# Kernel optimization log

Measured on AMD Instinct MI355X. Metric: run time of the kernel, lower is better.

The kernel has to match this reference:

```python
import jax, jax.numpy as jnp
import numpy as np

N = 100_000          # nodes
E = 1_600_000        # directed edges (before self-loops)
IN_DIM, H1, H2, H3 = 128, 64, 64, 64
NEG_SLOPE = 0.2      # PyG GATConv default


def setup_inputs() -> dict:
    key = jax.random.key(0)
    ks = jax.random.split(key, 20)

    def glorot(k, shape):
        fan = shape[0] + shape[-1] if len(shape) > 1 else 1 + shape[0]
        return jax.random.normal(k, shape, jnp.float32) * np.float32(np.sqrt(2.0 / fan))

    inp = {
        "x": jax.random.normal(ks[0], (N, IN_DIM), jnp.float32),
        "edge_index": jax.random.randint(ks[1], (2, E), 0, N, jnp.int32),
        "W1": glorot(ks[2], (IN_DIM, H1)), "a1s": glorot(ks[3], (H1,)), "a1d": glorot(ks[4], (H1,)), "b1": jnp.zeros((H1,), jnp.float32),
        "W2": glorot(ks[5], (H1, H2)),     "a2s": glorot(ks[6], (H2,)), "a2d": glorot(ks[7], (H2,)), "b2": jnp.zeros((H2,), jnp.float32),
        "W3": glorot(ks[8], (H2, H3)),     "a3s": glorot(ks[9], (H3,)), "a3d": glorot(ks[10], (H3,)), "b3": jnp.zeros((H3,), jnp.float32),
        "Wl": glorot(ks[11], (H3, 1)),     "bl": jnp.zeros((1,), jnp.float32),
    }
    return inp


def _gat_layer(x, src, dst, W, a_src, a_dst, b):
    # x: [N, Fin]; src/dst: [E'] (self-loops included)
    h = x @ W                              # [N, Fout]
    alpha_s = h @ a_src                    # [N]
    alpha_d = h @ a_dst                    # [N]
    e = jax.nn.leaky_relu(alpha_s[src] + alpha_d[dst], NEG_SLOPE)  # [E']
    # segment softmax over edges grouped by destination node
    m = jax.ops.segment_max(e, dst, num_segments=N)
    p = jnp.exp(e - m[dst])
    s = jax.ops.segment_sum(p, dst, num_segments=N)
    alpha = p / (s[dst] + 1e-16)           # [E']
    out = jax.ops.segment_sum(alpha[:, None] * h[src], dst, num_segments=N)  # [N, Fout]
    return out + b


def reference(x, edge_index, W1, a1s, a1d, b1, W2, a2s, a2d, b2, W3, a3s, a3d, b3, Wl, bl):
    # add self-loops (PyG GATConv default add_self_loops=True)
    loops = jnp.arange(N, dtype=edge_index.dtype)
    src = jnp.concatenate([edge_index[0], loops])
    dst = jnp.concatenate([edge_index[1], loops])

    h = jax.nn.relu(_gat_layer(x, src, dst, W1, a1s, a1d, b1))   # dropout is identity in eval
    h = jax.nn.relu(_gat_layer(h, src, dst, W2, a2s, a2d, b2))
    h = jax.nn.relu(_gat_layer(h, src, dst, W3, a3s, a3d, b3))
    return jax.nn.sigmoid(h @ Wl + bl)      # [N, 1]
```

## Files before the change

kernel.cpp:

```cpp
#include <hip/hip_runtime.h>
#include <hip/hip_bf16.h>
#include <math.h>

#define BSH 8
#define MAXBK 512
#define PCHUNK 4096

typedef __attribute__((ext_vector_type(8)))  short short8;
typedef __attribute__((ext_vector_type(16))) float f32x16;

__device__ __forceinline__ float half_reduce_max(float v) {
  #pragma unroll
  for (int off = 16; off; off >>= 1) v = fmaxf(v, __shfl_xor(v, off));
  return v;
}
__device__ __forceinline__ float half_reduce_sum(float v) {
  #pragma unroll
  for (int off = 16; off; off >>= 1) v += __shfl_xor(v, off);
  return v;
}

__device__ __forceinline__ unsigned f2bf(float f) {
  unsigned u = __float_as_uint(f);
  return (u + 0x7fffu + ((u >> 16) & 1u)) >> 16;
}
__device__ __forceinline__ float bf_lo(unsigned u) { return __uint_as_float(u << 16); }
__device__ __forceinline__ float bf_hi(unsigned u) { return __uint_as_float(u & 0xffff0000u); }

__device__ __forceinline__ void async_copy16(const void* gsrc, void* ldst) {
  __builtin_amdgcn_global_load_lds(
      (const __attribute__((address_space(1))) void*)gsrc,
      (__attribute__((address_space(3))) void*)ldst, 16, 0, 0);
}

__device__ __forceinline__ void wave0_excl_scan(unsigned* arr, unsigned* out, int n, int t) {
  if (t < 64) {
    unsigned carry = 0;
    for (int c = 0; c < n / 64; c++) {
      unsigned v = arr[c * 64 + t];
      unsigned s = v;
      #pragma unroll
      for (int off = 1; off < 64; off <<= 1) {
        unsigned u = __shfl_up(s, off);
        if ((t & 63) >= off) s += u;
      }
      out[c * 64 + t] = s - v + carry;
      carry += __shfl(s, 63);
    }
  }
}


__global__ __launch_bounds__(256) void k_bhist(const int* __restrict__ ei,
                                               unsigned* __restrict__ gbucket,
                                               int E, int EE, int nbk) {
  __shared__ unsigned hist[MAXBK];
  int t = threadIdx.x;
  for (int i = t; i < nbk; i += 256) hist[i] = 0;
  __syncthreads();
  for (int e = blockIdx.x * 256 + t; e < EE; e += gridDim.x * 256) {
    int d = (e < E) ? ei[E + e] : (e - E);
    atomicAdd(&hist[d >> BSH], 1u);
  }
  __syncthreads();
  for (int i = t; i < nbk; i += 256)
    if (hist[i]) atomicAdd(&gbucket[i], hist[i]);
}

__global__ __launch_bounds__(256) void k_bscan(const unsigned* __restrict__ gbucket,
                                               unsigned* __restrict__ bbase,
                                               unsigned* __restrict__ bfill,
                                               int nbk, int EE) {
  __shared__ unsigned arr[MAXBK], exc[MAXBK];
  int t = threadIdx.x;
  for (int i = t; i < MAXBK; i += 256) arr[i] = (i < nbk) ? gbucket[i] : 0u;
  __syncthreads();
  wave0_excl_scan(arr, exc, MAXBK, t);
  __syncthreads();
  for (int i = t; i < nbk; i += 256) { bbase[i] = exc[i]; bfill[i] = exc[i]; }
  if (t == 0) bbase[nbk] = (unsigned)EE;
}

__global__ __launch_bounds__(256) void k_part(const int* __restrict__ ei,
                                              unsigned* __restrict__ bfill,
                                              uint2* __restrict__ part,
                                              int E, int EE) {
  __shared__ uint2 stage[PCHUNK];
  __shared__ unsigned lcnt[MAXBK], lexcl[MAXBK], lbase[MAXBK];
  int t = threadIdx.x;
  int base = blockIdx.x * PCHUNK;
  int cnt = EE - base; if (cnt > PCHUNK) cnt = PCHUNK;
  for (int i = t; i < MAXBK; i += 256) lcnt[i] = 0;
  __syncthreads();

  uint2 ed[16]; unsigned loc[16];
  #pragma unroll
  for (int i = 0; i < 16; i++) {
    int e = base + i * 256 + t;
    if (e < EE) {
      int s, d;
      if (e < E) { s = ei[e]; d = ei[E + e]; } else { s = e - E; d = s; }
      ed[i] = make_uint2((unsigned)s, (unsigned)d);
      loc[i] = atomicAdd(&lcnt[(unsigned)d >> BSH], 1u);
    }
  }
  __syncthreads();
  wave0_excl_scan(lcnt, lexcl, MAXBK, t);
  __syncthreads();
  for (int i = t; i < MAXBK; i += 256) {
    unsigned c = lcnt[i];
    lbase[i] = c ? atomicAdd(&bfill[i], c) : 0u;
  }
  __syncthreads();
  #pragma unroll
  for (int i = 0; i < 16; i++) {
    int e = base + i * 256 + t;
    if (e < EE) stage[lexcl[ed[i].y >> BSH] + loc[i]] = ed[i];
  }
  __syncthreads();
  for (int i = t; i < cnt; i += 256) {
    uint2 v = stage[i];
    unsigned b = v.y >> BSH;
    part[lbase[b] + ((unsigned)i - lexcl[b])] = v;
  }
}

__global__ __launch_bounds__(256) void k_bcsr(const uint2* __restrict__ part,
                                              const unsigned* __restrict__ bbase,
                                              int* __restrict__ rowptr,
                                              int* __restrict__ csr_src,
                                              int Nn, int nbk) {
  __shared__ unsigned sdeg[256], sexcl[256], sfill[256];
  int t = threadIdx.x, b = blockIdx.x;
  int e0 = (int)bbase[b], e1 = (int)bbase[b + 1];
  sdeg[t] = 0; sfill[t] = 0;
  __syncthreads();
  for (int j = e0 + t; j < e1; j += 256)
    atomicAdd(&sdeg[part[j].y & 255u], 1u);
  __syncthreads();
  wave0_excl_scan(sdeg, sexcl, 256, t);
  __syncthreads();
  int node = (b << BSH) + t;
  if (node < Nn) rowptr[node] = e0 + (int)sexcl[t];
  if (b == nbk - 1 && t == 0) rowptr[Nn] = e1;
  for (int j = e0 + t; j < e1; j += 256) {
    uint2 v = part[j];
    unsigned dl = v.y & 255u;
    unsigned k = atomicAdd(&sfill[dl], 1u);
    csr_src[e0 + (int)sexcl[dl] + (int)k] = (int)v.x;
  }
}


__global__ __launch_bounds__(256) void k_wprep(const float* __restrict__ W1,
                                               const float* __restrict__ W2,
                                               const float* __restrict__ W3,
                                               short8* __restrict__ wf) {
  int idx = blockIdx.x * 256 + threadIdx.x;
  if (idx >= 2048) return;
  int g = idx >> 6, l = idx & 63;
  const float* W; int s, t;
  if (g < 16)      { W = W1; s = g >> 1;        t = g & 1; }
  else if (g < 24) { W = W2; s = (g - 16) >> 1; t = g & 1; }
  else             { W = W3; s = (g - 24) >> 1; t = g & 1; }
  int of = t * 32 + (l & 31);
  int k0 = s * 16 + (l >> 5) * 8;
  short8 v;
  #pragma unroll
  for (int e = 0; e < 8; e++) v[e] = (short)f2bf(W[(k0 + e) * 64 + of]);
  wf[idx] = v;
}


template <int K, bool F32IN>
__global__ __launch_bounds__(256) void k_gemm7(
    const void* __restrict__ xin, const short8* __restrict__ wf,
    const float* __restrict__ avs, const float* __restrict__ avd,
    unsigned* __restrict__ h, float* __restrict__ as_out,
    float* __restrict__ ad_out, int Nn) {
  constexpr int NS = K / 16;
  constexpr int RB = F32IN ? K * 4 : K * 2;
  constexpr int RSH = F32IN ? (K == 128 ? 9 : 8) : (K == 128 ? 8 : 7);
  __shared__ __align__(16) char xs_raw[128 * RB];
  int t = threadIdx.x, lane = t & 63, wid = t >> 6;
  int l31 = lane & 31, hi = lane >> 5;

  short8 wa[NS * 2];
  #pragma unroll
  for (int i = 0; i < NS * 2; i++) wa[i] = wf[i * 64 + lane];

  int tile0 = blockIdx.x * 128;
  const char* xg = (const char*)xin;
  constexpr int CH = (128 * RB) / (256 * 16);
  #pragma unroll
  for (int i = 0; i < CH; i++) {
    int off = (i * 256 + t) * 16;
    int row = off >> RSH;
    int inrow = off & (RB - 1);
    long grow = (long)tile0 + row;
    if (grow > (long)Nn - 1) grow = Nn - 1;
    async_copy16(xg + grow * RB + (inrow ^ ((row & 7) << 4)), xs_raw + off);
  }
  __syncthreads();

  f32x16 acc0 = {0,0,0,0,0,0,0,0,0,0,0,0,0,0,0,0};
  f32x16 acc1 = {0,0,0,0,0,0,0,0,0,0,0,0,0,0,0,0};
  int rowl = wid * 32 + l31;
  int swz = (rowl & 7) << 4;

  #pragma unroll
  for (int s = 0; s < NS; s++) {
    short8 bf;
    if constexpr (F32IN) {
      int ph = (rowl * RB + s * 64 + hi * 32) ^ swz;
      float4 fA = *(const float4*)(xs_raw + ph);
      float4 fB = *(const float4*)(xs_raw + (ph ^ 16));
      bf[0] = (short)f2bf(fA.x); bf[1] = (short)f2bf(fA.y);
      bf[2] = (short)f2bf(fA.z); bf[3] = (short)f2bf(fA.w);
      bf[4] = (short)f2bf(fB.x); bf[5] = (short)f2bf(fB.y);
      bf[6] = (short)f2bf(fB.z); bf[7] = (short)f2bf(fB.w);
    } else {
      int ph = (rowl * RB + s * 32 + hi * 16) ^ swz;
      bf = *(const short8*)(xs_raw + ph);
    }
    acc0 = __builtin_amdgcn_mfma_f32_32x32x16_bf16(wa[2 * s], bf, acc0, 0, 0, 0);
    acc1 = __builtin_amdgcn_mfma_f32_32x32x16_bf16(wa[2 * s + 1], bf, acc1, 0, 0, 0);
  }

  int xrow = tile0 + rowl;
  bool ok = xrow < Nn;
  float asp = 0.f, adp = 0.f;
  #pragma unroll
  for (int r = 0; r < 16; r += 2) {
    int rof = (r & 3) + 8 * (r >> 2);
    int of0 = rof + 4 * hi;
    if (ok) {
      h[(size_t)xrow * 32 + (of0 >> 1)] =
          (f2bf(acc0[r + 1]) << 16) | f2bf(acc0[r]);
      h[(size_t)xrow * 32 + 16 + (of0 >> 1)] =
          (f2bf(acc1[r + 1]) << 16) | f2bf(acc1[r]);
    }
    asp += acc0[r] * avs[of0] + acc0[r + 1] * avs[of0 + 1]
         + acc1[r] * avs[of0 + 32] + acc1[r + 1] * avs[of0 + 33];
    adp += acc0[r] * avd[of0] + acc0[r + 1] * avd[of0 + 1]
         + acc1[r] * avd[of0 + 32] + acc1[r + 1] * avd[of0 + 33];
  }
  asp += __shfl_xor(asp, 32);
  adp += __shfl_xor(adp, 32);
  if (ok && hi == 0) { as_out[xrow] = asp; ad_out[xrow] = adp; }
}


template <int FINAL>
__global__ __launch_bounds__(256) void k_agg8(
    const int* __restrict__ rowptr, const int* __restrict__ csr_src,
    const unsigned* __restrict__ hp, const float* __restrict__ as_,
    const float* __restrict__ ad_, const float* __restrict__ bias,
    unsigned* __restrict__ out, const float* __restrict__ Wlin,
    const float* __restrict__ blin, float* __restrict__ fout, int Nn) {
  __shared__ float2 psbuf[4][2][32];
  int t = threadIdx.x, lane = t & 63, wid = t >> 6;
  int fl = lane & 31, hh = lane >> 5;
  int n = blockIdx.x * 8 + wid * 2 + hh;
  bool valid = n < Nn;
  int nn = valid ? n : (Nn - 1);
  int r0 = rowptr[nn], r1 = rowptr[nn + 1];
  int deg = valid ? (r1 - r0) : 0;
  float ad = ad_[nn];

  if (deg <= 32) {
    int src = (fl < deg) ? csr_src[r0 + fl] : 0;
    float e = (fl < deg) ? (as_[src] + ad) : -3.0e38f;
    e = (e >= 0.f) ? e : 0.2f * e;
    float m = half_reduce_max(e);
    float p = (fl < deg) ? __expf(e - m) : 0.f;
    float inv = 1.f / (half_reduce_sum(p) + 1e-16f);
    psbuf[wid][hh][fl] = make_float2(p, __uint_as_float((unsigned)src * 128u));

    int sub = fl >> 4, q = fl & 15;
    const char* hq = (const char*)hp + q * 8;
    float a0 = 0.f, a1 = 0.f, a2 = 0.f, a3 = 0.f;
    float b0 = 0.f, b1 = 0.f, b2 = 0.f, b3 = 0.f;
    for (int jj = 0; jj < deg; jj += 4) {
      float2 ps0 = psbuf[wid][hh][jj + sub];
      float2 ps1 = psbuf[wid][hh][jj + 2 + sub];
      uint2 v0 = *(const uint2*)(hq + __float_as_uint(ps0.y));
      uint2 v1 = *(const uint2*)(hq + __float_as_uint(ps1.y));
      a0 = fmaf(ps0.x, bf_lo(v0.x), a0);
      a1 = fmaf(ps0.x, bf_hi(v0.x), a1);
      a2 = fmaf(ps0.x, bf_lo(v0.y), a2);
      a3 = fmaf(ps0.x, bf_hi(v0.y), a3);
      b0 = fmaf(ps1.x, bf_lo(v1.x), b0);
      b1 = fmaf(ps1.x, bf_hi(v1.x), b1);
      b2 = fmaf(ps1.x, bf_lo(v1.y), b2);
      b3 = fmaf(ps1.x, bf_hi(v1.y), b3);
    }
    a0 += b0; a1 += b1; a2 += b2; a3 += b3;
    a0 += __shfl_xor(a0, 16);
    a1 += __shfl_xor(a1, 16);
    a2 += __shfl_xor(a2, 16);
    a3 += __shfl_xor(a3, 16);

    float4 bi = ((const float4*)bias)[q];
    float o0 = fmaxf(fmaf(a0, inv, bi.x), 0.f);
    float o1 = fmaxf(fmaf(a1, inv, bi.y), 0.f);
    float o2 = fmaxf(fmaf(a2, inv, bi.z), 0.f);
    float o3 = fmaxf(fmaf(a3, inv, bi.w), 0.f);
    if (FINAL) {
      float4 wl = ((const float4*)Wlin)[q];
      float rv = (sub == 0) ? (o0 * wl.x + o1 * wl.y + o2 * wl.z + o3 * wl.w) : 0.f;
      rv = half_reduce_sum(rv);
      if (valid && fl == 0) {
        float z = rv + blin[0];
        fout[n] = 1.f / (1.f + __expf(-z));
      }
    } else if (valid && sub == 0) {
      uint2 pk;
      pk.x = (f2bf(o1) << 16) | f2bf(o0);
      pk.y = (f2bf(o3) << 16) | f2bf(o2);
      *(uint2*)(out + (size_t)n * 32 + 2 * q) = pk;
    }
  } else {
    float acc0 = 0.f, acc1 = 0.f;
    float m = -3.0e38f;
    for (int j = r0 + fl; j < r1; j += 32) {
      float e = as_[csr_src[j]] + ad;
      e = (e >= 0.f) ? e : 0.2f * e;
      m = fmaxf(m, e);
    }
    m = half_reduce_max(m);
    float ssum = 0.f;
    for (int j = r0; j < r1; ++j) {
      int src = csr_src[j];
      float e = as_[src] + ad;
      e = (e >= 0.f) ? e : 0.2f * e;
      float p = __expf(e - m);
      ssum += p;
      unsigned v = hp[(size_t)src * 32 + fl];
      acc0 = fmaf(p, bf_lo(v), acc0);
      acc1 = fmaf(p, bf_hi(v), acc1);
    }
    float inv2 = 1.f / (ssum + 1e-16f);
    acc0 *= inv2;
    acc1 *= inv2;
    float2 bi = ((const float2*)bias)[fl];
    float o0 = fmaxf(acc0 + bi.x, 0.f);
    float o1 = fmaxf(acc1 + bi.y, 0.f);
    if (FINAL) {
      float2 wl = ((const float2*)Wlin)[fl];
      float rv = half_reduce_sum(o0 * wl.x + o1 * wl.y);
      if (valid && fl == 0) {
        float z = rv + blin[0];
        fout[n] = 1.f / (1.f + __expf(-z));
      }
    } else {
      if (valid) out[(size_t)n * 32 + fl] = (f2bf(o1) << 16) | f2bf(o0);
    }
  }
}

extern "C" void kernel_launch(void* const* d_in, const int* in_sizes, int n_in,
                              void* d_out, int out_size, void* d_ws, size_t ws_size,
                              hipStream_t stream) {
  const float* x   = (const float*)d_in[0];
  const int*   ei  = (const int*)d_in[1];
  const float* W1  = (const float*)d_in[2];
  const float* a1s = (const float*)d_in[3];
  const float* a1d = (const float*)d_in[4];
  const float* b1  = (const float*)d_in[5];
  const float* W2  = (const float*)d_in[6];
  const float* a2s = (const float*)d_in[7];
  const float* a2d = (const float*)d_in[8];
  const float* b2  = (const float*)d_in[9];
  const float* W3  = (const float*)d_in[10];
  const float* a3s = (const float*)d_in[11];
  const float* a3d = (const float*)d_in[12];
  const float* b3  = (const float*)d_in[13];
  const float* Wl  = (const float*)d_in[14];
  const float* bl  = (const float*)d_in[15];

  const int N  = in_sizes[0] / 128;
  const int E  = in_sizes[1] / 2;
  const int EE = E + N;
  const int nbk = (N + 255) >> 8;

  char* p = (char*)d_ws;
  auto alloc = [&](size_t bytes) { char* r = p; p += (bytes + 255) & ~(size_t)255; return r; };
  unsigned* gbucket = (unsigned*)alloc((size_t)MAXBK * 4);
  unsigned* bbase   = (unsigned*)alloc((size_t)(MAXBK + 1) * 4);
  unsigned* bfill   = (unsigned*)alloc((size_t)MAXBK * 4);
  short8*   wf      = (short8*)alloc(2048 * 16);
  int*      rowptr  = (int*)alloc((size_t)(N + 1) * 4);
  int*      csr_src = (int*)alloc((size_t)EE * 4);
  unsigned* hbuf    = (unsigned*)alloc((size_t)N * 32 * 4);
  char*     regionA = alloc((size_t)EE * 8);
  float*    as_     = (float*)alloc((size_t)N * 4);
  float*    ad_     = (float*)alloc((size_t)N * 4);

  uint2*    part = (uint2*)regionA;
  unsigned* obuf = (unsigned*)regionA;

  hipMemsetAsync(gbucket, 0, (size_t)MAXBK * 4, stream);

  k_wprep<<<8, 256, 0, stream>>>(W1, W2, W3, wf);
  k_bhist<<<256, 256, 0, stream>>>(ei, gbucket, E, EE, nbk);
  k_bscan<<<1, 256, 0, stream>>>(gbucket, bbase, bfill, nbk, EE);
  k_part<<<(EE + PCHUNK - 1) / PCHUNK, 256, 0, stream>>>(ei, bfill, part, E, EE);
  k_bcsr<<<nbk, 256, 0, stream>>>(part, bbase, rowptr, csr_src, N, nbk);

  int gb = (N + 127) / 128;
  int nb = (N + 7) / 8;

  k_gemm7<128, true><<<gb, 256, 0, stream>>>(x, wf, a1s, a1d, hbuf, as_, ad_, N);
  k_agg8<0><<<nb, 256, 0, stream>>>(rowptr, csr_src, hbuf, as_, ad_, b1, obuf,
                                    nullptr, nullptr, nullptr, N);
  k_gemm7<64, false><<<gb, 256, 0, stream>>>(obuf, wf + 16 * 64, a2s, a2d,
                                             hbuf, as_, ad_, N);
  k_agg8<0><<<nb, 256, 0, stream>>>(rowptr, csr_src, hbuf, as_, ad_, b2, obuf,
                                    nullptr, nullptr, nullptr, N);
  k_gemm7<64, false><<<gb, 256, 0, stream>>>(obuf, wf + 24 * 64, a3s, a3d,
                                             hbuf, as_, ad_, N);
  k_agg8<1><<<nb, 256, 0, stream>>>(rowptr, csr_src, hbuf, as_, ad_, b3, nullptr,
                                    Wl, bl, (float*)d_out, N);
}
```

Before: 256.5 us.

## Vectorize histogram, stage bucket edges in LDS, software-pipeline aggregation gathers

The bucket histogram now reads destination indices as int4 and adds the self-loop counts analytically in the scan instead of iterating over them. The CSR build caches each bucket's edges in shared memory so the second pass avoids re-reading global memory, falling back to the old path when a bucket overflows the cap. The aggregation loop is software-pipelined to issue the next gathers before the current FMAs. The large LDS buffer may lower occupancy of k_bcsr, and the pipelined loop reads psbuf entries past deg, which rely on the zeroed padding in the buffer.

```diff
diff --git a/kernel.cpp b/kernel.cpp
--- a/kernel.cpp
+++ b/kernel.cpp
@@ -5,6 +5,7 @@
 #define BSH 8
 #define MAXBK 512
 #define PCHUNK 4096
+#define BCSR_CAP 6144
 
 typedef __attribute__((ext_vector_type(8)))  short short8;
 typedef __attribute__((ext_vector_type(16))) float f32x16;
@@ -53,14 +54,23 @@
 
 __global__ __launch_bounds__(256) void k_bhist(const int* __restrict__ ei,
                                                unsigned* __restrict__ gbucket,
-                                               int E, int EE, int nbk) {
+                                               int E, int nbk) {
   __shared__ unsigned hist[MAXBK];
   int t = threadIdx.x;
   for (int i = t; i < nbk; i += 256) hist[i] = 0;
   __syncthreads();
-  for (int e = blockIdx.x * 256 + t; e < EE; e += gridDim.x * 256) {
-    int d = (e < E) ? ei[E + e] : (e - E);
-    atomicAdd(&hist[d >> BSH], 1u);
+  const int4* d4 = (const int4*)(ei + E);
+  int nd4 = E >> 2;
+  for (int i = blockIdx.x * 256 + t; i < nd4; i += gridDim.x * 256) {
+    int4 d = d4[i];
+    atomicAdd(&hist[d.x >> BSH], 1u);
+    atomicAdd(&hist[d.y >> BSH], 1u);
+    atomicAdd(&hist[d.z >> BSH], 1u);
+    atomicAdd(&hist[d.w >> BSH], 1u);
+  }
+  if (blockIdx.x == 0) {
+    for (int e = (nd4 << 2) + t; e < E; e += 256)
+      atomicAdd(&hist[ei[E + e] >> BSH], 1u);
   }
   __syncthreads();
   for (int i = t; i < nbk; i += 256)
@@ -70,10 +80,18 @@
 __global__ __launch_bounds__(256) void k_bscan(const unsigned* __restrict__ gbucket,
                                                unsigned* __restrict__ bbase,
                                                unsigned* __restrict__ bfill,
-                                               int nbk, int EE) {
+                                               int nbk, int EE, int Nn) {
   __shared__ unsigned arr[MAXBK], exc[MAXBK];
   int t = threadIdx.x;
-  for (int i = t; i < MAXBK; i += 256) arr[i] = (i < nbk) ? gbucket[i] : 0u;
+  for (int i = t; i < MAXBK; i += 256) {
+    unsigned v = 0;
+    if (i < nbk) {
+      int rem = Nn - (i << BSH);
+      unsigned sl = rem >= 256 ? 256u : (unsigned)(rem > 0 ? rem : 0);
+      v = gbucket[i] + sl;
+    }
+    arr[i] = v;
+  }
   __syncthreads();
   wave0_excl_scan(arr, exc, MAXBK, t);
   __syncthreads();
@@ -131,23 +149,43 @@
                                               int* __restrict__ csr_src,
                                               int Nn, int nbk) {
   __shared__ unsigned sdeg[256], sexcl[256], sfill[256];
+  __shared__ uint2 epart[BCSR_CAP];
   int t = threadIdx.x, b = blockIdx.x;
   int e0 = (int)bbase[b], e1 = (int)bbase[b + 1];
+  int cnt = e1 - e0;
+  bool fits = cnt <= BCSR_CAP;
   sdeg[t] = 0; sfill[t] = 0;
   __syncthreads();
-  for (int j = e0 + t; j < e1; j += 256)
-    atomicAdd(&sdeg[part[j].y & 255u], 1u);
+  if (fits) {
+    for (int j = t; j < cnt; j += 256) {
+      uint2 v = part[e0 + j];
+      epart[j] = v;
+      atomicAdd(&sdeg[v.y & 255u], 1u);
+    }
+  } else {
+    for (int j = e0 + t; j < e1; j += 256)
+      atomicAdd(&sdeg[part[j].y & 255u], 1u);
+  }
   __syncthreads();
   wave0_excl_scan(sdeg, sexcl, 256, t);
   __syncthreads();
   int node = (b << BSH) + t;
   if (node < Nn) rowptr[node] = e0 + (int)sexcl[t];
   if (b == nbk - 1 && t == 0) rowptr[Nn] = e1;
-  for (int j = e0 + t; j < e1; j += 256) {
-    uint2 v = part[j];
-    unsigned dl = v.y & 255u;
-    unsigned k = atomicAdd(&sfill[dl], 1u);
-    csr_src[e0 + (int)sexcl[dl] + (int)k] = (int)v.x;
+  if (fits) {
+    for (int j = t; j < cnt; j += 256) {
+      uint2 v = epart[j];
+      unsigned dl = v.y & 255u;
+      unsigned k = atomicAdd(&sfill[dl], 1u);
+      csr_src[e0 + (int)sexcl[dl] + (int)k] = (int)v.x;
+    }
+  } else {
+    for (int j = e0 + t; j < e1; j += 256) {
+      uint2 v = part[j];
+      unsigned dl = v.y & 255u;
+      unsigned k = atomicAdd(&sfill[dl], 1u);
+      csr_src[e0 + (int)sexcl[dl] + (int)k] = (int)v.x;
+    }
   }
 }
 
@@ -252,7 +290,7 @@
 
 
 template <int FINAL>
-__global__ __launch_bounds__(256) void k_agg8(
+__global__ __launch_bounds__(256) void k_agg9(
     const int* __restrict__ rowptr, const int* __restrict__ csr_src,
     const unsigned* __restrict__ hp, const float* __restrict__ as_,
     const float* __restrict__ ad_, const float* __restrict__ bias,
@@ -279,13 +317,19 @@
 
     int sub = fl >> 4, q = fl & 15;
     const char* hq = (const char*)hp + q * 8;
+    const float2* psb = psbuf[wid][hh];
     float a0 = 0.f, a1 = 0.f, a2 = 0.f, a3 = 0.f;
     float b0 = 0.f, b1 = 0.f, b2 = 0.f, b3 = 0.f;
-    for (int jj = 0; jj < deg; jj += 4) {
-      float2 ps0 = psbuf[wid][hh][jj + sub];
-      float2 ps1 = psbuf[wid][hh][jj + 2 + sub];
-      uint2 v0 = *(const uint2*)(hq + __float_as_uint(ps0.y));
-      uint2 v1 = *(const uint2*)(hq + __float_as_uint(ps1.y));
+
+    float2 ps0 = psb[sub];
+    float2 ps1 = psb[2 + sub];
+    uint2 v0 = *(const uint2*)(hq + __float_as_uint(ps0.y));
+    uint2 v1 = *(const uint2*)(hq + __float_as_uint(ps1.y));
+    for (int jj = 4; jj < deg; jj += 4) {
+      float2 nps0 = psb[jj + sub];
+      float2 nps1 = psb[jj + 2 + sub];
+      uint2 nv0 = *(const uint2*)(hq + __float_as_uint(nps0.y));
+      uint2 nv1 = *(const uint2*)(hq + __float_as_uint(nps1.y));
       a0 = fmaf(ps0.x, bf_lo(v0.x), a0);
       a1 = fmaf(ps0.x, bf_hi(v0.x), a1);
       a2 = fmaf(ps0.x, bf_lo(v0.y), a2);
@@ -294,7 +338,17 @@
       b1 = fmaf(ps1.x, bf_hi(v1.x), b1);
       b2 = fmaf(ps1.x, bf_lo(v1.y), b2);
       b3 = fmaf(ps1.x, bf_hi(v1.y), b3);
-    }
+      ps0 = nps0; ps1 = nps1; v0 = nv0; v1 = nv1;
+    }
+    a0 = fmaf(ps0.x, bf_lo(v0.x), a0);
+    a1 = fmaf(ps0.x, bf_hi(v0.x), a1);
+    a2 = fmaf(ps0.x, bf_lo(v0.y), a2);
+    a3 = fmaf(ps0.x, bf_hi(v0.y), a3);
+    b0 = fmaf(ps1.x, bf_lo(v1.x), b0);
+    b1 = fmaf(ps1.x, bf_hi(v1.x), b1);
+    b2 = fmaf(ps1.x, bf_lo(v1.y), b2);
+    b3 = fmaf(ps1.x, bf_hi(v1.y), b3);
+
     a0 += b0; a1 += b1; a2 += b2; a3 += b3;
     a0 += __shfl_xor(a0, 16);
     a1 += __shfl_xor(a1, 16);
@@ -403,8 +457,8 @@
   hipMemsetAsync(gbucket, 0, (size_t)MAXBK * 4, stream);
 
   k_wprep<<<8, 256, 0, stream>>>(W1, W2, W3, wf);
-  k_bhist<<<256, 256, 0, stream>>>(ei, gbucket, E, EE, nbk);
-  k_bscan<<<1, 256, 0, stream>>>(gbucket, bbase, bfill, nbk, EE);
+  k_bhist<<<256, 256, 0, stream>>>(ei, gbucket, E, nbk);
+  k_bscan<<<1, 256, 0, stream>>>(gbucket, bbase, bfill, nbk, EE, N);
   k_part<<<(EE + PCHUNK - 1) / PCHUNK, 256, 0, stream>>>(ei, bfill, part, E, EE);
   k_bcsr<<<nbk, 256, 0, stream>>>(part, bbase, rowptr, csr_src, N, nbk);
 
@@ -412,14 +466,14 @@
   int nb = (N + 7) / 8;
 
   k_gemm7<128, true><<<gb, 256, 0, stream>>>(x, wf, a1s, a1d, hbuf, as_, ad_, N);
-  k_agg8<0><<<nb, 256, 0, stream>>>(rowptr, csr_src, hbuf, as_, ad_, b1, obuf,
+  k_agg9<0><<<nb, 256, 0, stream>>>(rowptr, csr_src, hbuf, as_, ad_, b1, obuf,
                                     nullptr, nullptr, nullptr, N);
   k_gemm7<64, false><<<gb, 256, 0, stream>>>(obuf, wf + 16 * 64, a2s, a2d,
                                              hbuf, as_, ad_, N);
-  k_agg8<0><<<nb, 256, 0, stream>>>(rowptr, csr_src, hbuf, as_, ad_, b2, obuf,
+  k_agg9<0><<<nb, 256, 0, stream>>>(rowptr, csr_src, hbuf, as_, ad_, b2, obuf,
                                     nullptr, nullptr, nullptr, N);
   k_gemm7<64, false><<<gb, 256, 0, stream>>>(obuf, wf + 24 * 64, a3s, a3d,
                                              hbuf, as_, ad_, N);
-  k_agg8<1><<<nb, 256, 0, stream>>>(rowptr, csr_src, hbuf, as_, ad_, b3, nullptr,
+  k_agg9<1><<<nb, 256, 0, stream>>>(rowptr, csr_src, hbuf, as_, ad_, b3, nullptr,
                                     Wl, bl, (float*)d_out, N);
 }
```

Result: no change. 252.4 us (-1.6%).
